# Kernel tuning notes

Measured on AMD Instinct MI355X. Metric: run time of the kernel, lower is better.

## Reference

```python
import jax, jax.numpy as jnp
import numpy as np

N = 50000
E = 800000
D = 64  # in = hidden = out channels


def _graph_conv(x, src, dst, ew, W_rel, b_rel, W_root, b_root, num_nodes):
    # PyG GraphConv: out = lin_rel(scatter_add(x[src] * w -> dst)) + lin_root(x)
    msg = x[src] * ew[:, None]                      # [E, d_in] edge-wise gather
    agg = jax.ops.segment_sum(msg, dst, num_segments=num_nodes)  # scatter-add
    return agg @ W_rel.T + b_rel + x @ W_root.T + b_root


def setup_inputs() -> dict:
    key = jax.random.key(0)
    ks = jax.random.split(key, 16)
    s = 0.05
    inp = {
        "X": jax.random.normal(ks[0], (N, D), dtype=jnp.float32),
        "edge_index": jax.random.randint(ks[1], (2, E), 0, N, dtype=jnp.int64),
        "edge_weight": jax.random.uniform(ks[2], (E,), dtype=jnp.float32),
        # conv_whx_x: in -> hidden
        "Wrel1": jax.random.normal(ks[3], (D, D), dtype=jnp.float32) * s,
        "brel1": jax.random.normal(ks[4], (D,), dtype=jnp.float32) * s,
        "Wroot1": jax.random.normal(ks[5], (D, D), dtype=jnp.float32) * s,
        "broot1": jax.random.normal(ks[6], (D,), dtype=jnp.float32) * s,
        # conv_whh_hs1: hidden -> hidden
        "Wrel2": jax.random.normal(ks[7], (D, D), dtype=jnp.float32) * s,
        "brel2": jax.random.normal(ks[8], (D,), dtype=jnp.float32) * s,
        "Wroot2": jax.random.normal(ks[9], (D, D), dtype=jnp.float32) * s,
        "broot2": jax.random.normal(ks[10], (D,), dtype=jnp.float32) * s,
        # conv_wy_y: hidden -> out
        "Wrel3": jax.random.normal(ks[11], (D, D), dtype=jnp.float32) * s,
        "brel3": jax.random.normal(ks[12], (D,), dtype=jnp.float32) * s,
        "Wroot3": jax.random.normal(ks[13], (D, D), dtype=jnp.float32) * s,
        "broot3": jax.random.normal(ks[14], (D,), dtype=jnp.float32) * s,
    }
    return inp


def reference(X, edge_index, edge_weight,
              Wrel1, brel1, Wroot1, broot1,
              Wrel2, brel2, Wroot2, broot2,
              Wrel3, brel3, Wroot3, broot3):
    num_nodes = X.shape[0]
    src, dst = edge_index[0], edge_index[1]
    # first call: hidden state H_{t-1} = zeros(N, out_channels)
    H_prev = jnp.zeros((num_nodes, D), dtype=X.dtype)
    Whx_x = _graph_conv(X, src, dst, edge_weight, Wrel1, brel1, Wroot1, broot1, num_nodes)
    Whh_h = _graph_conv(H_prev, src, dst, edge_weight, Wrel2, brel2, Wroot2, broot2, num_nodes)
    H = jax.nn.sigmoid(Whx_x + Whh_h)
    Wy_h = _graph_conv(H, src, dst, edge_weight, Wrel3, brel3, Wroot3, broot3, num_nodes)
    return jax.nn.sigmoid(Wy_h)
```

## Files before the change

### kernel.cpp

```cpp
#include <hip/hip_runtime.h>

#define D 64
#define CAP 64

typedef unsigned short u16;
typedef unsigned int u32;
typedef short bf16x8 __attribute__((ext_vector_type(8)));
typedef float f32x4 __attribute__((ext_vector_type(4)));

__device__ __forceinline__ u16 f2bf(float f) {
    u32 u = __float_as_uint(f);
    return (u16)((u + 0x7FFFu + ((u >> 16) & 1u)) >> 16);
}

__global__ void k_prep(const float* __restrict__ X, u16* __restrict__ Xbf,
                       int* __restrict__ cnt, int n4, int N,
                       const float* __restrict__ Wrel1, const float* __restrict__ Wroot1,
                       const float* __restrict__ Wrel3, const float* __restrict__ Wroot3,
                       const float* __restrict__ brel1, const float* __restrict__ broot1,
                       const float* __restrict__ brel2, const float* __restrict__ broot2,
                       const float* __restrict__ brel3, const float* __restrict__ broot3,
                       u16* __restrict__ Wpk, float* __restrict__ Bpk) {
    int i = blockIdx.x * blockDim.x + threadIdx.x;
    if (i < N) cnt[i] = 0;

    if (i < 2048) {
        int f    = i >> 6;
        int lane = i & 63;
        int stage = f >> 4, rest = f & 15;
        int mat = rest >> 3, t = (rest >> 1) & 3, kk = rest & 1;
        int ml = lane & 15, ql = lane >> 4;
        const float* W = stage ? (mat ? Wroot3 : Wrel3) : (mat ? Wroot1 : Wrel1);
        const float* src = W + (t * 16 + ml) * D + kk * 32 + ql * 8;
        union { u16 h[8]; uint4 v; } o;
#pragma unroll
        for (int e = 0; e < 8; ++e) o.h[e] = f2bf(src[e]);
        *reinterpret_cast<uint4*>(Wpk + (size_t)(f * 64 + lane) * 8) = o.v;
    }
    if (i < 128) {
        int stage = i >> 6, c = i & 63;
        Bpk[i] = stage ? (brel3[c] + broot3[c])
                       : (brel1[c] + broot1[c] + brel2[c] + broot2[c]);
    }

    if (i >= n4) return;
    float4 v = reinterpret_cast<const float4*>(X)[i];
    ushort4 o;
    o.x = f2bf(v.x); o.y = f2bf(v.y); o.z = f2bf(v.z); o.w = f2bf(v.w);
    reinterpret_cast<ushort4*>(Xbf)[i] = o;
}

__global__ void k_fill(const int* __restrict__ ei, const float* __restrict__ ew,
                       int* __restrict__ cnt, u32* __restrict__ pairs,
                       int E, int step) {
    const int g  = blockIdx.x & 7;
    const int b  = blockIdx.x >> 3;
    const int lo = g * step;
    const int hi = lo + step;
    const int nthr = (gridDim.x >> 3) * blockDim.x;
    const int t  = b * blockDim.x + threadIdx.x;
    const int nchunk = E >> 2;

    for (int c = t; c < nchunk; c += nthr) {
        int e = c * 4;
        int4 d4 = *reinterpret_cast<const int4*>(ei + E + e);
#define DO_EDGE(dd, kk)                                                          \
        if ((dd) >= lo && (dd) < hi) {                                           \
            int p = atomicAdd(cnt + (dd), 1);                                    \
            if (p < CAP)                                                         \
                pairs[(dd) * CAP + p] =                                          \
                    (((u32)f2bf(ew[e + kk])) << 16) | (u32)ei[e + kk];           \
        }
        DO_EDGE(d4.x, 0)
        DO_EDGE(d4.y, 1)
        DO_EDGE(d4.z, 2)
        DO_EDGE(d4.w, 3)
#undef DO_EDGE
    }
    if (g == 0 && t == 0) {
        for (int e = nchunk * 4; e < E; ++e) {
            int d = ei[E + e];
            int p = atomicAdd(cnt + d, 1);
            if (p < CAP) pairs[d * CAP + p] = (((u32)f2bf(ew[e])) << 16) | (u32)ei[e];
        }
    }
}

template <int STAGE>
__global__ __launch_bounds__(256, 3) void k_stage(
        const u16* __restrict__ Gbf,
        const u16* __restrict__ Wpk,
        const float* __restrict__ Bpk,
        const int* __restrict__ cnt, const u32* __restrict__ pairs,
        float* __restrict__ outF, u16* __restrict__ outBf, int N) {
    __shared__ __align__(16) u16 smem[4 * 8 * 72];
    const int lane = threadIdx.x & 63;
    const int wid  = threadIdx.x >> 6;
    const int ml   = lane & 15;
    const int ql   = lane >> 4;
    const int hq   = lane & 15;
    const int n0   = blockIdx.x * 32 + wid * 8;
    u16* sw = smem + wid * 8 * 72;

    if (n0 >= N) return;

    int cidx = n0 + (lane & 7); if (cidx >= N) cidx = N - 1;
    const int cnt8 = cnt[cidx];

    int deg[8], degmax = 0;
#pragma unroll
    for (int i = 0; i < 8; ++i) {
        int d = (n0 + i < N) ? __builtin_amdgcn_readlane(cnt8, i) : 0;
        if (d > CAP) d = CAP;
        deg[i] = d;
        degmax = degmax > d ? degmax : d;
    }

    u32 pp[8];
#pragma unroll
    for (int i = 0; i < 8; ++i) {
        int r = n0 + i; if (r >= N) r = N - 1;
        pp[i] = (lane < deg[i]) ? pairs[(size_t)r * CAP + lane] : 0u;
    }

    const bool qb0 = (ql & 1) != 0;
    const bool qb1 = (ql & 2) != 0;
    const int  hq8 = hq * 8;
    const char* gbase = (const char*)Gbf;

    f32x4 acc[2];
#pragma unroll
    for (int p = 0; p < 2; ++p) acc[p] = (f32x4){0.f, 0.f, 0.f, 0.f};

    uint2 vA[4][2], vB[4][2], vC[4][2];
    u32   wA[4][2], wB[4][2], wC[4][2];
#define ISSUE(vbuf, wbuf, jj)                                                   \
    _Pragma("unroll") for (int s = 0; s < 4; ++s)                               \
    _Pragma("unroll") for (int p = 0; p < 2; ++p) {                             \
        u32 r0 = (u32)__builtin_amdgcn_readlane((int)pp[4 * p + 0], (jj) + s);  \
        u32 r1 = (u32)__builtin_amdgcn_readlane((int)pp[4 * p + 1], (jj) + s);  \
        u32 r2 = (u32)__builtin_amdgcn_readlane((int)pp[4 * p + 2], (jj) + s);  \
        u32 r3 = (u32)__builtin_amdgcn_readlane((int)pp[4 * p + 3], (jj) + s);  \
        u32 c01 = qb0 ? r1 : r0;                                                \
        u32 c23 = qb0 ? r3 : r2;                                                \
        u32 sel = qb1 ? c23 : c01;                                              \
        wbuf[s][p] = sel;                                                       \
        vbuf[s][p] = *(const uint2*)(gbase + ((size_t)(sel & 0xFFFFu) << 7) + hq8); \
    }
#define CONSUME(vbuf, wbuf)                                                     \
    _Pragma("unroll") for (int s = 0; s < 4; ++s)                               \
    _Pragma("unroll") for (int p = 0; p < 2; ++p) {                             \
        float w  = __uint_as_float(wbuf[s][p] & 0xFFFF0000u);                   \
        uint2 d  = vbuf[s][p];                                                  \
        acc[p][0] = fmaf(w, __uint_as_float(d.x << 16),         acc[p][0]);     \
        acc[p][1] = fmaf(w, __uint_as_float(d.x & 0xFFFF0000u), acc[p][1]);     \
        acc[p][2] = fmaf(w, __uint_as_float(d.y << 16),         acc[p][2]);     \
        acc[p][3] = fmaf(w, __uint_as_float(d.y & 0xFFFF0000u), acc[p][3]);     \
    }

    if (degmax > 0) {
        int j = 0;
        ISSUE(vA, wA, 0)
        if (4 < degmax) ISSUE(vB, wB, 4)
        for (;;) {
            if (j + 8 < degmax) ISSUE(vC, wC, j + 8)
            CONSUME(vA, wA)
            j += 4;
            if (j >= degmax) break;
            if (j + 8 < degmax) ISSUE(vA, wA, j + 8)
            CONSUME(vB, wB)
            j += 4;
            if (j >= degmax) break;
            if (j + 8 < degmax) ISSUE(vB, wB, j + 8)
            CONSUME(vC, wC)
            j += 4;
            if (j >= degmax) break;
        }
    }
#undef ISSUE
#undef CONSUME

#pragma unroll
    for (int p = 0; p < 2; ++p) {
        uint2 packed;
        packed.x = ((u32)f2bf(acc[p][1]) << 16) | (u32)f2bf(acc[p][0]);
        packed.y = ((u32)f2bf(acc[p][3]) << 16) | (u32)f2bf(acc[p][2]);
        int row = 4 * p + ql;
        *reinterpret_cast<uint2*>(sw + row * 72 + hq * 4) = packed;
    }

    bf16x8 brel[4][2], broot[4][2];
#pragma unroll
    for (int t = 0; t < 4; ++t)
#pragma unroll
        for (int kk = 0; kk < 2; ++kk) {
            brel[t][kk]  = *reinterpret_cast<const bf16x8*>(Wpk + (size_t)(((0 * 4 + t) * 2 + kk) * 64 + lane) * 8);
            broot[t][kk] = *reinterpret_cast<const bf16x8*>(Wpk + (size_t)(((1 * 4 + t) * 2 + kk) * 64 + lane) * 8);
        }

    const int am = ml & 7;
    bf16x8 a_agg[2], a_x[2];
#pragma unroll
    for (int kk = 0; kk < 2; ++kk)
        a_agg[kk] = *reinterpret_cast<bf16x8*>(sw + am * 72 + kk * 32 + ql * 8);
    {
        int r = n0 + am; if (r >= N) r = N - 1;
#pragma unroll
        for (int kk = 0; kk < 2; ++kk)
            a_x[kk] = *reinterpret_cast<const bf16x8*>(Gbf + (size_t)r * D + kk * 32 + ql * 8);
    }

#pragma unroll
    for (int t = 0; t < 4; ++t) {
        int c = t * 16 + ml;
        float bias = Bpk[c];

        f32x4 accv = {0.f, 0.f, 0.f, 0.f};
        accv = __builtin_amdgcn_mfma_f32_16x16x32_bf16(a_agg[0], brel[t][0],  accv, 0, 0, 0);
        accv = __builtin_amdgcn_mfma_f32_16x16x32_bf16(a_agg[1], brel[t][1],  accv, 0, 0, 0);
        accv = __builtin_amdgcn_mfma_f32_16x16x32_bf16(a_x[0],   broot[t][0], accv, 0, 0, 0);
        accv = __builtin_amdgcn_mfma_f32_16x16x32_bf16(a_x[1],   broot[t][1], accv, 0, 0, 0);
        if (ql < 2) {
#pragma unroll
            for (int r = 0; r < 4; ++r) {
                int row = n0 + ql * 4 + r;
                if (row < N) {
                    float z = accv[r] + bias;
                    float h = 1.f / (1.f + __expf(-z));
                    int off = row * D + c;
                    if (STAGE == 1) outBf[off] = f2bf(h);
                    else            outF[off]  = h;
                }
            }
        }
    }
}

extern "C" void kernel_launch(void* const* d_in, const int* in_sizes, int n_in,
                              void* d_out, int out_size, void* d_ws, size_t ws_size,
                              hipStream_t stream) {
    const float* X      = (const float*)d_in[0];
    const int*   ei     = (const int*)  d_in[1];
    const float* ew     = (const float*)d_in[2];
    const float* Wrel1  = (const float*)d_in[3];
    const float* brel1  = (const float*)d_in[4];
    const float* Wroot1 = (const float*)d_in[5];
    const float* broot1 = (const float*)d_in[6];
    const float* brel2  = (const float*)d_in[8];
    const float* broot2 = (const float*)d_in[10];
    const float* Wrel3  = (const float*)d_in[11];
    const float* brel3  = (const float*)d_in[12];
    const float* Wroot3 = (const float*)d_in[13];
    const float* broot3 = (const float*)d_in[14];

    const int N = in_sizes[0] / D;
    const int E = in_sizes[1] / 2;

    char* ws = (char*)d_ws;
    int* cnt = (int*)ws;
    size_t off = (((size_t)N * 4) + 255) & ~(size_t)255;
    u32* pairs = (u32*)(ws + off);        off += (size_t)N * CAP * 4;
    u16* Xbf   = (u16*)(ws + off);        off += (size_t)N * D * 2;
    u16* Hbf   = (u16*)(ws + off);        off += (size_t)N * D * 2;
    u16* Wpk   = (u16*)(ws + off);        off += (size_t)32 * 64 * 8 * 2;
    float* Bpk = (float*)(ws + off);

    {
        int n4 = N * D / 4;
        int T  = n4 > N ? n4 : N;
        k_prep<<<(T + 255) / 256, 256, 0, stream>>>(
            X, Xbf, cnt, n4, N, Wrel1, Wroot1, Wrel3, Wroot3,
            brel1, broot1, brel2, broot2, brel3, broot3, Wpk, Bpk);
    }
    {
        int step = (N + 7) / 8;
        k_fill<<<1600, 256, 0, stream>>>(ei, ew, cnt, pairs, E, step);
    }

    const int NB = (N + 31) / 32;
    k_stage<1><<<NB, 256, 0, stream>>>(Xbf, Wpk, Bpk,
                                       cnt, pairs, nullptr, Hbf, N);
    k_stage<2><<<NB, 256, 0, stream>>>(Hbf, Wpk + 16 * 64 * 8, Bpk + 64,
                                       cnt, pairs, (float*)d_out, nullptr, N);
}
```

Baseline: 198.8 us.

## Fuse prep and CSR fill into one kernel, remap stage blocks per XCD

```diff
diff --git a/kernel.cpp b/kernel.cpp
--- a/kernel.cpp
+++ b/kernel.cpp
@@ -2,6 +2,7 @@
 
 #define D 64
 #define CAP 64
+#define FILLB 1600
 
 typedef unsigned short u16;
 typedef unsigned int u32;
@@ -13,75 +14,79 @@
     return (u16)((u + 0x7FFFu + ((u >> 16) & 1u)) >> 16);
 }
 
-__global__ void k_prep(const float* __restrict__ X, u16* __restrict__ Xbf,
-                       int* __restrict__ cnt, int n4, int N,
+__global__ void k_work(const int* __restrict__ ei, const float* __restrict__ ew,
+                       int* __restrict__ cnt, u32* __restrict__ pairs, int E,
+                       const float* __restrict__ X, u16* __restrict__ Xbf, int n4,
                        const float* __restrict__ Wrel1, const float* __restrict__ Wroot1,
                        const float* __restrict__ Wrel3, const float* __restrict__ Wroot3,
                        const float* __restrict__ brel1, const float* __restrict__ broot1,
                        const float* __restrict__ brel2, const float* __restrict__ broot2,
                        const float* __restrict__ brel3, const float* __restrict__ broot3,
                        u16* __restrict__ Wpk, float* __restrict__ Bpk) {
-    int i = blockIdx.x * blockDim.x + threadIdx.x;
-    if (i < N) cnt[i] = 0;
-
-    if (i < 2048) {
-        int f    = i >> 6;
-        int lane = i & 63;
-        int stage = f >> 4, rest = f & 15;
-        int mat = rest >> 3, t = (rest >> 1) & 3, kk = rest & 1;
-        int ml = lane & 15, ql = lane >> 4;
-        const float* W = stage ? (mat ? Wroot3 : Wrel3) : (mat ? Wroot1 : Wrel1);
-        const float* src = W + (t * 16 + ml) * D + kk * 32 + ql * 8;
-        union { u16 h[8]; uint4 v; } o;
-#pragma unroll
-        for (int e = 0; e < 8; ++e) o.h[e] = f2bf(src[e]);
-        *reinterpret_cast<uint4*>(Wpk + (size_t)(f * 64 + lane) * 8) = o.v;
-    }
-    if (i < 128) {
-        int stage = i >> 6, c = i & 63;
-        Bpk[i] = stage ? (brel3[c] + broot3[c])
-                       : (brel1[c] + broot1[c] + brel2[c] + broot2[c]);
-    }
-
-    if (i >= n4) return;
-    float4 v = reinterpret_cast<const float4*>(X)[i];
-    ushort4 o;
-    o.x = f2bf(v.x); o.y = f2bf(v.y); o.z = f2bf(v.z); o.w = f2bf(v.w);
-    reinterpret_cast<ushort4*>(Xbf)[i] = o;
-}
-
-__global__ void k_fill(const int* __restrict__ ei, const float* __restrict__ ew,
-                       int* __restrict__ cnt, u32* __restrict__ pairs,
-                       int E, int step) {
-    const int g  = blockIdx.x & 7;
-    const int b  = blockIdx.x >> 3;
-    const int lo = g * step;
-    const int hi = lo + step;
-    const int nthr = (gridDim.x >> 3) * blockDim.x;
-    const int t  = b * blockDim.x + threadIdx.x;
-    const int nchunk = E >> 2;
-
-    for (int c = t; c < nchunk; c += nthr) {
-        int e = c * 4;
-        int4 d4 = *reinterpret_cast<const int4*>(ei + E + e);
+    if (blockIdx.x < FILLB) {
+        const int g  = blockIdx.x & 7;
+        const int b  = blockIdx.x >> 3;
+        const int step = 6250;
+        const int lo = g * step;
+        const int hi = (g == 7) ? 0x7FFFFFFF : lo + step;
+        const int nthr = (FILLB >> 3) * blockDim.x;
+        const int t  = b * blockDim.x + threadIdx.x;
+        const int nchunk = E >> 2;
+
+        for (int c = t; c < nchunk; c += nthr) {
+            int e = c * 4;
+            int4 d4 = *reinterpret_cast<const int4*>(ei + E + e);
 #define DO_EDGE(dd, kk)                                                          \
-        if ((dd) >= lo && (dd) < hi) {                                           \
-            int p = atomicAdd(cnt + (dd), 1);                                    \
-            if (p < CAP)                                                         \
-                pairs[(dd) * CAP + p] =                                          \
-                    (((u32)f2bf(ew[e + kk])) << 16) | (u32)ei[e + kk];           \
-        }
-        DO_EDGE(d4.x, 0)
-        DO_EDGE(d4.y, 1)
-        DO_EDGE(d4.z, 2)
-        DO_EDGE(d4.w, 3)
+            if ((dd) >= lo && (dd) < hi) {                                       \
+                int p = atomicAdd(cnt + (dd), 1);                                \
+                if (p < CAP)                                                     \
+                    pairs[(dd) * CAP + p] =                                      \
+                        (((u32)f2bf(ew[e + kk])) << 16) | (u32)ei[e + kk];       \
+            }
+            DO_EDGE(d4.x, 0)
+            DO_EDGE(d4.y, 1)
+            DO_EDGE(d4.z, 2)
+            DO_EDGE(d4.w, 3)
 #undef DO_EDGE
-    }
-    if (g == 0 && t == 0) {
-        for (int e = nchunk * 4; e < E; ++e) {
-            int d = ei[E + e];
-            int p = atomicAdd(cnt + d, 1);
-            if (p < CAP) pairs[d * CAP + p] = (((u32)f2bf(ew[e])) << 16) | (u32)ei[e];
+        }
+        if (g == 0 && t == 0) {
+            for (int e = nchunk * 4; e < E; ++e) {
+                int d = ei[E + e];
+                int p = atomicAdd(cnt + d, 1);
+                if (p < CAP) pairs[d * CAP + p] = (((u32)f2bf(ew[e])) << 16) | (u32)ei[e];
+            }
+        }
+    } else {
+        int tid = (blockIdx.x - FILLB) * blockDim.x + threadIdx.x;
+
+        if (tid < 2048) {
+            int f    = tid >> 6;
+            int lane = tid & 63;
+            int stage = f >> 4, rest = f & 15;
+            int mat = rest >> 3, t = (rest >> 1) & 3, kk = rest & 1;
+            int ml = lane & 15, ql = lane >> 4;
+            const float* W = stage ? (mat ? Wroot3 : Wrel3) : (mat ? Wroot1 : Wrel1);
+            const float* src = W + (t * 16 + ml) * D + kk * 32 + ql * 8;
+            union { u16 h[8]; uint4 v; } o;
+#pragma unroll
+            for (int e = 0; e < 8; ++e) o.h[e] = f2bf(src[e]);
+            *reinterpret_cast<uint4*>(Wpk + (size_t)(f * 64 + lane) * 8) = o.v;
+        }
+        if (tid < 128) {
+            int stage = tid >> 6, c = tid & 63;
+            Bpk[tid] = stage ? (brel3[c] + broot3[c])
+                             : (brel1[c] + broot1[c] + brel2[c] + broot2[c]);
+        }
+
+        int xi = tid * 4;
+#pragma unroll
+        for (int k = 0; k < 4; ++k) {
+            if (xi + k < n4) {
+                float4 v = reinterpret_cast<const float4*>(X)[xi + k];
+                ushort4 o;
+                o.x = f2bf(v.x); o.y = f2bf(v.y); o.z = f2bf(v.z); o.w = f2bf(v.w);
+                reinterpret_cast<ushort4*>(Xbf)[xi + k] = o;
+            }
         }
     }
 }
@@ -92,14 +97,15 @@
         const u16* __restrict__ Wpk,
         const float* __restrict__ Bpk,
         const int* __restrict__ cnt, const u32* __restrict__ pairs,
-        float* __restrict__ outF, u16* __restrict__ outBf, int N) {
+        float* __restrict__ outF, u16* __restrict__ outBf, int N, int P) {
     __shared__ __align__(16) u16 smem[4 * 8 * 72];
     const int lane = threadIdx.x & 63;
     const int wid  = threadIdx.x >> 6;
     const int ml   = lane & 15;
     const int ql   = lane >> 4;
     const int hq   = lane & 15;
-    const int n0   = blockIdx.x * 32 + wid * 8;
+    const int lb   = (blockIdx.x & 7) * P + (blockIdx.x >> 3);
+    const int n0   = lb * 32 + wid * 8;
     u16* sw = smem + wid * 8 * 72;
 
     if (n0 >= N) return;
@@ -120,7 +126,9 @@
 #pragma unroll
     for (int i = 0; i < 8; ++i) {
         int r = n0 + i; if (r >= N) r = N - 1;
-        pp[i] = (lane < deg[i]) ? pairs[(size_t)r * CAP + lane] : 0u;
+        pp[i] = (lane < deg[i])
+                    ? __builtin_nontemporal_load(pairs + (size_t)r * CAP + lane)
+                    : 0u;
     }
 
     const bool qb0 = (ql & 1) != 0;
@@ -265,21 +273,21 @@
     u16* Wpk   = (u16*)(ws + off);        off += (size_t)32 * 64 * 8 * 2;
     float* Bpk = (float*)(ws + off);
 
+    hipMemsetAsync(cnt, 0, (size_t)N * 4, stream);
+
     {
         int n4 = N * D / 4;
-        int T  = n4 > N ? n4 : N;
-        k_prep<<<(T + 255) / 256, 256, 0, stream>>>(
-            X, Xbf, cnt, n4, N, Wrel1, Wroot1, Wrel3, Wroot3,
+        int prepB = (n4 + 1023) / 1024;
+        k_work<<<FILLB + prepB, 256, 0, stream>>>(
+            ei, ew, cnt, pairs, E, X, Xbf, n4,
+            Wrel1, Wroot1, Wrel3, Wroot3,
             brel1, broot1, brel2, broot2, brel3, broot3, Wpk, Bpk);
     }
-    {
-        int step = (N + 7) / 8;
-        k_fill<<<1600, 256, 0, stream>>>(ei, ew, cnt, pairs, E, step);
-    }
-
-    const int NB = (N + 31) / 32;
-    k_stage<1><<<NB, 256, 0, stream>>>(Xbf, Wpk, Bpk,
-                                       cnt, pairs, nullptr, Hbf, N);
-    k_stage<2><<<NB, 256, 0, stream>>>(Hbf, Wpk + 16 * 64 * 8, Bpk + 64,
-                                       cnt, pairs, (float*)d_out, nullptr, N);
-}
+
+    const int NBL = (N + 31) / 32;
+    const int P   = (NBL + 7) / 8;
+    k_stage<1><<<8 * P, 256, 0, stream>>>(Xbf, Wpk, Bpk,
+                                          cnt, pairs, nullptr, Hbf, N, P);
+    k_stage<2><<<8 * P, 256, 0, stream>>>(Hbf, Wpk + 16 * 64 * 8, Bpk + 64,
+                                          cnt, pairs, (float*)d_out, nullptr, N, P);
+}
```

Result: no change. 199.2 us (+0.2%).
